# Optimization experiments

Hardware: AMD Instinct MI355X
Metric: run time of the kernel (lower is better)

The kernel has to match this reference:

```python
import jax, jax.numpy as jnp
import numpy as np

SIGMA = 1.0
TOP_K = 4

def setup_inputs() -> dict:
    key = jax.random.key(0)
    k1, k2, k3, k4 = jax.random.split(key, 4)
    B, N, IN_DIM, OUT_DIM, P = 2, 4096, 128, 128, 3
    x = jax.random.normal(k1, (B, N, IN_DIM), dtype=jnp.float32)
    pos = jax.random.normal(k2, (B, N, P), dtype=jnp.float32)
    # Linear(in_dim, out_dim): W [in_dim, out_dim], b [out_dim]
    lim = 1.0 / np.sqrt(IN_DIM)
    W = jax.random.uniform(k3, (IN_DIM, OUT_DIM), minval=-lim, maxval=lim, dtype=jnp.float32)
    b = jax.random.uniform(k4, (OUT_DIM,), minval=-lim, maxval=lim, dtype=jnp.float32)
    return {"x": x, "pos": pos, "W": W, "b": b}

def reference(x, pos, W, b):
    B, N, _ = x.shape
    # pairwise distances [B, N, N]
    pos_diff = pos[:, :, None, :] - pos[:, None, :, :]
    dist = jnp.sqrt(jnp.sum(pos_diff ** 2, axis=-1) + 1e-8)
    adj = jnp.exp(-dist ** 2 / (2.0 * SIGMA ** 2))
    # top-k mask along last dim
    _, indices = jax.lax.top_k(adj, TOP_K)  # [B, N, k]
    b_idx = jnp.arange(B)[:, None, None]
    n_idx = jnp.arange(N)[None, :, None]
    mask = jnp.zeros_like(adj).at[b_idx, n_idx, indices].set(1.0)
    adj = adj * mask
    adj = adj / (jnp.sum(adj, axis=-1, keepdims=True) + 1e-8)
    # weighted aggregation + linear
    out = jnp.einsum('bnm,bmd->bnd', adj, x)
    return out @ W + b
```

## Files before the change

kernel.cpp:

```cpp
#include <hip/hip_runtime.h>
#include <hip/hip_bf16.h>

#define NPTS 4096
#define NROWS 8192
#define DIM 128
#define GEMM_BLOCKS 1024
#define HCELL 0.25f
#define LOW (-4.0f)
#define CAP 16
#define NCELLS 32768
#define OVCAP 4096

typedef __attribute__((ext_vector_type(8))) short bf16x8;
typedef __attribute__((ext_vector_type(4))) float f32x4;

__device__ __forceinline__ int cellcoord(float v) {
    int c = (int)floorf((v - LOW) / HCELL);
    return c < 0 ? 0 : (c > 31 ? 31 : c);
}

__global__ __launch_bounds__(256) void k1_gemm_bin(const float* __restrict__ x,
        const float* __restrict__ pos, const float* __restrict__ W,
        __hip_bfloat16* __restrict__ xWb, unsigned* __restrict__ cellCnt,
        float4* __restrict__ cellPts, unsigned* __restrict__ ovfCnt,
        float4* __restrict__ ovfList) {
    int b = blockIdx.x;
    if (b >= GEMM_BLOCKS) {
        int t = (b - GEMM_BLOCKS) * 256 + threadIdx.x;
        int batch = t >> 12;
        const float* p = pos + (size_t)t * 3;
        float px = p[0], py = p[1], pz = p[2];
        int cx = cellcoord(px), cy = cellcoord(py), cz = cellcoord(pz);
        int cid = ((batch * 32 + cz) * 32 + cy) * 32 + cx;
        unsigned slot = atomicAdd(&cellCnt[cid], 1u);
        float4 rec = make_float4(px, py, pz, __uint_as_float((unsigned)(t & (NPTS - 1))));
        if (slot < CAP) cellPts[(size_t)cid * CAP + slot] = rec;
        else { unsigned o = atomicAdd(&ovfCnt[batch], 1u);
               if (o < OVCAP) ovfList[(size_t)batch * OVCAP + o] = rec; }
        return;
    }
    int wave = threadIdx.x >> 6, lane = threadIdx.x & 63;
    int tile = b * 4 + wave;
    int m0 = (tile >> 3) << 4, n0 = (tile & 7) << 4;
    int r = lane & 15, kg = lane >> 4;
    const float* xr = x + (size_t)(m0 + r) * DIM + kg * 8;
    const float* wc = W + (size_t)(kg * 8) * DIM + (n0 + r);
    f32x4 acc = {0.f, 0.f, 0.f, 0.f};
    union { __hip_bfloat16 h; short s; } u;
#pragma unroll
    for (int kb = 0; kb < 4; ++kb) {
        float4 a0 = *(const float4*)(xr + kb * 32);
        float4 a1 = *(const float4*)(xr + kb * 32 + 4);
        bf16x8 af, bf;
        u.h = __float2bfloat16(a0.x); af[0] = u.s;
        u.h = __float2bfloat16(a0.y); af[1] = u.s;
        u.h = __float2bfloat16(a0.z); af[2] = u.s;
        u.h = __float2bfloat16(a0.w); af[3] = u.s;
        u.h = __float2bfloat16(a1.x); af[4] = u.s;
        u.h = __float2bfloat16(a1.y); af[5] = u.s;
        u.h = __float2bfloat16(a1.z); af[6] = u.s;
        u.h = __float2bfloat16(a1.w); af[7] = u.s;
#pragma unroll
        for (int i = 0; i < 8; ++i) {
            u.h = __float2bfloat16(wc[(size_t)(kb * 32 + i) * DIM]);
            bf[i] = u.s;
        }
        acc = __builtin_amdgcn_mfma_f32_16x16x32_bf16(af, bf, acc, 0, 0, 0);
    }
    int col = n0 + r, rbase = m0 + (kg << 2);
#pragma unroll
    for (int reg = 0; reg < 4; ++reg)
        xWb[(size_t)(rbase + reg) * DIM + col] = __float2bfloat16(acc[reg]);
}

__device__ __forceinline__ double mkkey(float d2, int j) {
    return __longlong_as_double(__double_as_longlong((double)d2) |
                                (unsigned long long)(unsigned)j);
}
__device__ __forceinline__ void kins(double& k0, double& k1, double& k2,
                                     double& k3, double s) {
    double c = fmax(k0, s); k0 = fmin(k0, s);
    double t = fmax(k1, c); k1 = fmin(k1, c); c = t;
    t = fmax(k2, c);        k2 = fmin(k2, c); c = t;
    k3 = fmin(k3, c);
}
__device__ __forceinline__ void kmerge(double& a0, double& a1, double& a2,
                                       double& a3, double b0, double b1,
                                       double b2, double b3) {
    double m0 = fmin(a0, b3), m1 = fmin(a1, b2);
    double m2 = fmin(a2, b1), m3 = fmin(a3, b0);
    double t0 = fmin(m0, m2), t2 = fmax(m0, m2);
    double t1 = fmin(m1, m3), t3 = fmax(m1, m3);
    a0 = fmin(t0, t1); a1 = fmax(t0, t1);
    a2 = fmin(t2, t3); a3 = fmax(t2, t3);
}

__global__ __launch_bounds__(256) void knn_agg(const unsigned* __restrict__ cellCnt,
        const float4* __restrict__ cellPts, const unsigned* __restrict__ ovfCnt,
        const float4* __restrict__ ovfList, const float* __restrict__ pos,
        const __hip_bfloat16* __restrict__ xWb, const float* __restrict__ bias,
        float* __restrict__ out) {
    int lane = threadIdx.x & 63;
    int wave = threadIdx.x >> 6;
    int row = blockIdx.x * 4 + wave;
    int batch = row >> 12;
    int qi = row & (NPTS - 1);
    const float* pb = pos + (size_t)batch * NPTS * 3;
    float qx = pb[3 * qi], qy = pb[3 * qi + 1], qz = pb[3 * qi + 2];
    int cx = cellcoord(qx), cy = cellcoord(qy), cz = cellcoord(qz);
    const unsigned* cb = cellCnt + (size_t)batch * NCELLS;
    const float4* pb4 = cellPts + (size_t)batch * NCELLS * CAP;

    const double INF = __builtin_inf();
    double k0 = INF, k1 = INF, k2 = INF, k3 = INF;

#pragma unroll
    for (int mm = 0; mm < 2; ++mm) {
        int m = lane + mm * 64;
        if (m < 125) {
            int dz = m / 25 - 2, dy = (m / 5) % 5 - 2, dx = m % 5 - 2;
            int nx = cx + dx, ny = cy + dy, nz = cz + dz;
            if ((unsigned)nx < 32u && (unsigned)ny < 32u && (unsigned)nz < 32u) {
                int lid = (nz * 32 + ny) * 32 + nx;
                unsigned c = cb[lid]; c = c < CAP ? c : CAP;
                const float4* cp = pb4 + (size_t)lid * CAP;
                for (unsigned s = 0; s < c; ++s) {
                    float4 p = cp[s];
                    float ddx = qx - p.x, ddy = qy - p.y, ddz = qz - p.z;
                    float d2 = fmaf(ddx, ddx, fmaf(ddy, ddy, ddz * ddz));
                    kins(k0, k1, k2, k3, mkkey(d2, (int)__float_as_uint(p.w)));
                }
            }
        }
    }
#pragma unroll
    for (int off = 1; off < 64; off <<= 1) {
        double p0 = __shfl_xor(k0, off), p1 = __shfl_xor(k1, off);
        double p2 = __shfl_xor(k2, off), p3 = __shfl_xor(k3, off);
        kmerge(k0, k1, k2, k3, p0, p1, p2, p3);
    }

    float dbox = 1e30f;
    if (cx - 2 > 0)  dbox = fminf(dbox, qx - (LOW + (cx - 2) * HCELL));
    if (cx + 2 < 31) dbox = fminf(dbox, (LOW + (cx + 3) * HCELL) - qx);
    if (cy - 2 > 0)  dbox = fminf(dbox, qy - (LOW + (cy - 2) * HCELL));
    if (cy + 2 < 31) dbox = fminf(dbox, (LOW + (cy + 3) * HCELL) - qy);
    if (cz - 2 > 0)  dbox = fminf(dbox, qz - (LOW + (cz - 2) * HCELL));
    if (cz + 2 < 31) dbox = fminf(dbox, (LOW + (cz + 3) * HCELL) - qz);
    bool resolved = ((float)k3 < 0.999f * dbox * dbox) && ((float)k3 < 1e29f);

    if (!resolved) {
        k0 = INF; k1 = INF; k2 = INF; k3 = INF;
#pragma unroll 4
        for (int t = 0; t < NPTS / 64; ++t) {
            int j = t * 64 + lane;
            float px = pb[3 * j], py = pb[3 * j + 1], pz = pb[3 * j + 2];
            float ddx = qx - px, ddy = qy - py, ddz = qz - pz;
            float d2 = fmaf(ddx, ddx, fmaf(ddy, ddy, ddz * ddz));
            kins(k0, k1, k2, k3, mkkey(d2, j));
        }
#pragma unroll
        for (int off = 1; off < 64; off <<= 1) {
            double p0 = __shfl_xor(k0, off), p1 = __shfl_xor(k1, off);
            double p2 = __shfl_xor(k2, off), p3 = __shfl_xor(k3, off);
            kmerge(k0, k1, k2, k3, p0, p1, p2, p3);
        }
    } else {
        unsigned oc = ovfCnt[batch]; oc = oc < OVCAP ? oc : OVCAP;
        const float4* ol = ovfList + (size_t)batch * OVCAP;
        for (unsigned o = 0; o < oc; ++o) {
            float4 p = ol[o];
            float ddx = qx - p.x, ddy = qy - p.y, ddz = qz - p.z;
            float d2 = fmaf(ddx, ddx, fmaf(ddy, ddy, ddz * ddz));
            kins(k0, k1, k2, k3, mkkey(d2, (int)__float_as_uint(p.w)));
        }
    }

    unsigned i0 = (unsigned)__double_as_longlong(k0) & 0xFFFu;
    unsigned i1 = (unsigned)__double_as_longlong(k1) & 0xFFFu;
    unsigned i2 = (unsigned)__double_as_longlong(k2) & 0xFFFu;
    unsigned i3 = (unsigned)__double_as_longlong(k3) & 0xFFFu;
    float d0 = (float)k0, d1 = (float)k1, d2 = (float)k2, d3 = (float)k3;
    float w0 = __expf(-(d0 + 1e-8f) * 0.5f);
    float w1 = __expf(-(d1 + 1e-8f) * 0.5f);
    float w2 = __expf(-(d2 + 1e-8f) * 0.5f);
    float w3 = __expf(-(d3 + 1e-8f) * 0.5f);
    float inv = 1.0f / (w0 + w1 + w2 + w3 + 1e-8f);
    w0 *= inv; w1 *= inv; w2 *= inv; w3 *= inv;
    int c = lane << 1;
    float2 bb = *(const float2*)(bias + c);
    const unsigned short* xu = (const unsigned short*)xWb;
    size_t bbase = ((size_t)batch * NPTS) << 7;
    ushort2 g0 = *(const ushort2*)(xu + bbase + ((size_t)i0 << 7) + c);
    ushort2 g1 = *(const ushort2*)(xu + bbase + ((size_t)i1 << 7) + c);
    ushort2 g2 = *(const ushort2*)(xu + bbase + ((size_t)i2 << 7) + c);
    ushort2 g3 = *(const ushort2*)(xu + bbase + ((size_t)i3 << 7) + c);
    float ox = bb.x + w0 * __uint_as_float((unsigned)g0.x << 16)
                    + w1 * __uint_as_float((unsigned)g1.x << 16)
                    + w2 * __uint_as_float((unsigned)g2.x << 16)
                    + w3 * __uint_as_float((unsigned)g3.x << 16);
    float oy = bb.y + w0 * __uint_as_float((unsigned)g0.y << 16)
                    + w1 * __uint_as_float((unsigned)g1.y << 16)
                    + w2 * __uint_as_float((unsigned)g2.y << 16)
                    + w3 * __uint_as_float((unsigned)g3.y << 16);
    *(float2*)(out + ((size_t)row << 7) + c) = make_float2(ox, oy);
}

extern "C" void kernel_launch(void* const* d_in, const int* in_sizes, int n_in,
                              void* d_out, int out_size, void* d_ws, size_t ws_size,
                              hipStream_t stream) {
    const float* x    = (const float*)d_in[0];
    const float* pos  = (const float*)d_in[1];
    const float* W    = (const float*)d_in[2];
    const float* bias = (const float*)d_in[3];
    float* out = (float*)d_out;

    char* ws = (char*)d_ws;
    __hip_bfloat16* xWb = (__hip_bfloat16*)ws;
    unsigned* cellCnt  = (unsigned*)(ws + 2097152);
    unsigned* ovfCnt   = (unsigned*)(ws + 2359296);
    float4* cellPts    = (float4*)(ws + 2359312);
    float4* ovfList    = (float4*)(ws + 2359312 + 16777216);

    hipMemsetAsync(ws + 2097152, 0, 262160, stream);
    k1_gemm_bin<<<GEMM_BLOCKS + NROWS / 256, 256, 0, stream>>>(
        x, pos, W, xWb, cellCnt, cellPts, ovfCnt, ovfList);
    knn_agg<<<NROWS / 4, 256, 0, stream>>>(
        cellCnt, cellPts, ovfCnt, ovfList, pos, xWb, bias, out);
}
```

Before: 84.27 us.

## Assign one block per query row and split cell scans across threads

The kNN kernel now processes one query row per 256-thread block instead of one per wave. Each of the 125 neighbour cells is split across two threads (half a cell each), with an inner loop unrolled by four, and per-wave top-4 results are merged through shared memory. This is meant to shorten the serial per-lane cell scan and expose more parallelism, at the cost of four times more blocks, two __syncthreads per merge, and half the threads idle in the output gather. The brute-force fallback is spread over 256 threads.

```diff
diff --git a/kernel.cpp b/kernel.cpp
--- a/kernel.cpp
+++ b/kernel.cpp
@@ -95,14 +95,37 @@
     a2 = fmin(t2, t3); a3 = fmax(t2, t3);
 }
 
+__device__ __forceinline__ void wave_bfly(double& k0, double& k1,
+                                          double& k2, double& k3) {
+#pragma unroll
+    for (int off = 1; off < 64; off <<= 1) {
+        double p0 = __shfl_xor(k0, off), p1 = __shfl_xor(k1, off);
+        double p2 = __shfl_xor(k2, off), p3 = __shfl_xor(k3, off);
+        kmerge(k0, k1, k2, k3, p0, p1, p2, p3);
+    }
+}
+
+__device__ __forceinline__ void block_merge(double (*sk)[4], int wave, int lane,
+                                            double& k0, double& k1,
+                                            double& k2, double& k3) {
+    __syncthreads();
+    if (lane == 0) { sk[wave][0] = k0; sk[wave][1] = k1;
+                     sk[wave][2] = k2; sk[wave][3] = k3; }
+    __syncthreads();
+    k0 = sk[0][0]; k1 = sk[0][1]; k2 = sk[0][2]; k3 = sk[0][3];
+    kmerge(k0, k1, k2, k3, sk[1][0], sk[1][1], sk[1][2], sk[1][3]);
+    kmerge(k0, k1, k2, k3, sk[2][0], sk[2][1], sk[2][2], sk[2][3]);
+    kmerge(k0, k1, k2, k3, sk[3][0], sk[3][1], sk[3][2], sk[3][3]);
+}
+
 __global__ __launch_bounds__(256) void knn_agg(const unsigned* __restrict__ cellCnt,
         const float4* __restrict__ cellPts, const unsigned* __restrict__ ovfCnt,
         const float4* __restrict__ ovfList, const float* __restrict__ pos,
         const __hip_bfloat16* __restrict__ xWb, const float* __restrict__ bias,
         float* __restrict__ out) {
-    int lane = threadIdx.x & 63;
-    int wave = threadIdx.x >> 6;
-    int row = blockIdx.x * 4 + wave;
+    int t = threadIdx.x;
+    int lane = t & 63, wave = t >> 6;
+    int row = blockIdx.x;
     int batch = row >> 12;
     int qi = row & (NPTS - 1);
     const float* pb = pos + (size_t)batch * NPTS * 3;
@@ -111,34 +134,47 @@
     const unsigned* cb = cellCnt + (size_t)batch * NCELLS;
     const float4* pb4 = cellPts + (size_t)batch * NCELLS * CAP;
 
+    __shared__ double sk[4][4];
+
     const double INF = __builtin_inf();
     double k0 = INF, k1 = INF, k2 = INF, k3 = INF;
 
-#pragma unroll
-    for (int mm = 0; mm < 2; ++mm) {
-        int m = lane + mm * 64;
-        if (m < 125) {
-            int dz = m / 25 - 2, dy = (m / 5) % 5 - 2, dx = m % 5 - 2;
-            int nx = cx + dx, ny = cy + dy, nz = cz + dz;
-            if ((unsigned)nx < 32u && (unsigned)ny < 32u && (unsigned)nz < 32u) {
-                int lid = (nz * 32 + ny) * 32 + nx;
-                unsigned c = cb[lid]; c = c < CAP ? c : CAP;
-                const float4* cp = pb4 + (size_t)lid * CAP;
-                for (unsigned s = 0; s < c; ++s) {
-                    float4 p = cp[s];
-                    float ddx = qx - p.x, ddy = qy - p.y, ddz = qz - p.z;
-                    float d2 = fmaf(ddx, ddx, fmaf(ddy, ddy, ddz * ddz));
-                    kins(k0, k1, k2, k3, mkkey(d2, (int)__float_as_uint(p.w)));
-                }
+    int m = t >> 1, h = t & 1;
+    if (m < 125) {
+        int dz = m / 25 - 2, dy = (m / 5) % 5 - 2, dx = m % 5 - 2;
+        int nx = cx + dx, ny = cy + dy, nz = cz + dz;
+        if ((unsigned)nx < 32u && (unsigned)ny < 32u && (unsigned)nz < 32u) {
+            int lid = (nz * 32 + ny) * 32 + nx;
+            unsigned c = cb[lid]; c = c < CAP ? c : CAP;
+            int lo = h << 3;
+            int hi = (int)c < lo + 8 ? (int)c : lo + 8;
+            const float4* cp = pb4 + (size_t)lid * CAP;
+            int s = lo;
+            for (; s + 3 < hi; s += 4) {
+                float4 p0 = cp[s], p1 = cp[s + 1], p2 = cp[s + 2], p3 = cp[s + 3];
+                float dx0 = qx - p0.x, dy0 = qy - p0.y, dz0 = qz - p0.z;
+                float dx1 = qx - p1.x, dy1 = qy - p1.y, dz1 = qz - p1.z;
+                float dx2 = qx - p2.x, dy2 = qy - p2.y, dz2 = qz - p2.z;
+                float dx3 = qx - p3.x, dy3 = qy - p3.y, dz3 = qz - p3.z;
+                float e0 = fmaf(dx0, dx0, fmaf(dy0, dy0, dz0 * dz0));
+                float e1 = fmaf(dx1, dx1, fmaf(dy1, dy1, dz1 * dz1));
+                float e2 = fmaf(dx2, dx2, fmaf(dy2, dy2, dz2 * dz2));
+                float e3 = fmaf(dx3, dx3, fmaf(dy3, dy3, dz3 * dz3));
+                kins(k0, k1, k2, k3, mkkey(e0, (int)__float_as_uint(p0.w)));
+                kins(k0, k1, k2, k3, mkkey(e1, (int)__float_as_uint(p1.w)));
+                kins(k0, k1, k2, k3, mkkey(e2, (int)__float_as_uint(p2.w)));
+                kins(k0, k1, k2, k3, mkkey(e3, (int)__float_as_uint(p3.w)));
             }
-        }
-    }
-#pragma unroll
-    for (int off = 1; off < 64; off <<= 1) {
-        double p0 = __shfl_xor(k0, off), p1 = __shfl_xor(k1, off);
-        double p2 = __shfl_xor(k2, off), p3 = __shfl_xor(k3, off);
-        kmerge(k0, k1, k2, k3, p0, p1, p2, p3);
-    }
+            for (; s < hi; ++s) {
+                float4 p = cp[s];
+                float ddx = qx - p.x, ddy = qy - p.y, ddz = qz - p.z;
+                float d2 = fmaf(ddx, ddx, fmaf(ddy, ddy, ddz * ddz));
+                kins(k0, k1, k2, k3, mkkey(d2, (int)__float_as_uint(p.w)));
+            }
+        }
+    }
+    wave_bfly(k0, k1, k2, k3);
+    block_merge(sk, wave, lane, k0, k1, k2, k3);
 
     float dbox = 1e30f;
     if (cx - 2 > 0)  dbox = fminf(dbox, qx - (LOW + (cx - 2) * HCELL));
@@ -152,19 +188,15 @@
     if (!resolved) {
         k0 = INF; k1 = INF; k2 = INF; k3 = INF;
 #pragma unroll 4
-        for (int t = 0; t < NPTS / 64; ++t) {
-            int j = t * 64 + lane;
+        for (int it = 0; it < NPTS / 256; ++it) {
+            int j = (it << 8) + t;
             float px = pb[3 * j], py = pb[3 * j + 1], pz = pb[3 * j + 2];
             float ddx = qx - px, ddy = qy - py, ddz = qz - pz;
             float d2 = fmaf(ddx, ddx, fmaf(ddy, ddy, ddz * ddz));
             kins(k0, k1, k2, k3, mkkey(d2, j));
         }
-#pragma unroll
-        for (int off = 1; off < 64; off <<= 1) {
-            double p0 = __shfl_xor(k0, off), p1 = __shfl_xor(k1, off);
-            double p2 = __shfl_xor(k2, off), p3 = __shfl_xor(k3, off);
-            kmerge(k0, k1, k2, k3, p0, p1, p2, p3);
-        }
+        wave_bfly(k0, k1, k2, k3);
+        block_merge(sk, wave, lane, k0, k1, k2, k3);
     } else {
         unsigned oc = ovfCnt[batch]; oc = oc < OVCAP ? oc : OVCAP;
         const float4* ol = ovfList + (size_t)batch * OVCAP;
@@ -187,23 +219,16 @@
     float w3 = __expf(-(d3 + 1e-8f) * 0.5f);
     float inv = 1.0f / (w0 + w1 + w2 + w3 + 1e-8f);
     w0 *= inv; w1 *= inv; w2 *= inv; w3 *= inv;
-    int c = lane << 1;
-    float2 bb = *(const float2*)(bias + c);
-    const unsigned short* xu = (const unsigned short*)xWb;
-    size_t bbase = ((size_t)batch * NPTS) << 7;
-    ushort2 g0 = *(const ushort2*)(xu + bbase + ((size_t)i0 << 7) + c);
-    ushort2 g1 = *(const ushort2*)(xu + bbase + ((size_t)i1 << 7) + c);
-    ushort2 g2 = *(const ushort2*)(xu + bbase + ((size_t)i2 << 7) + c);
-    ushort2 g3 = *(const ushort2*)(xu + bbase + ((size_t)i3 << 7) + c);
-    float ox = bb.x + w0 * __uint_as_float((unsigned)g0.x << 16)
-                    + w1 * __uint_as_float((unsigned)g1.x << 16)
-                    + w2 * __uint_as_float((unsigned)g2.x << 16)
-                    + w3 * __uint_as_float((unsigned)g3.x << 16);
-    float oy = bb.y + w0 * __uint_as_float((unsigned)g0.y << 16)
-                    + w1 * __uint_as_float((unsigned)g1.y << 16)
-                    + w2 * __uint_as_float((unsigned)g2.y << 16)
-                    + w3 * __uint_as_float((unsigned)g3.y << 16);
-    *(float2*)(out + ((size_t)row << 7) + c) = make_float2(ox, oy);
+    if (t < DIM) {
+        const unsigned short* xu = (const unsigned short*)xWb;
+        size_t bbase = ((size_t)batch * NPTS) << 7;
+        float g0 = __uint_as_float((unsigned)xu[bbase + ((size_t)i0 << 7) + t] << 16);
+        float g1 = __uint_as_float((unsigned)xu[bbase + ((size_t)i1 << 7) + t] << 16);
+        float g2 = __uint_as_float((unsigned)xu[bbase + ((size_t)i2 << 7) + t] << 16);
+        float g3 = __uint_as_float((unsigned)xu[bbase + ((size_t)i3 << 7) + t] << 16);
+        out[((size_t)row << 7) + t] =
+            bias[t] + w0 * g0 + w1 * g1 + w2 * g2 + w3 * g3;
+    }
 }
 
 extern "C" void kernel_launch(void* const* d_in, const int* in_sizes, int n_in,
@@ -225,6 +250,6 @@
     hipMemsetAsync(ws + 2097152, 0, 262160, stream);
     k1_gemm_bin<<<GEMM_BLOCKS + NROWS / 256, 256, 0, stream>>>(
         x, pos, W, xWb, cellCnt, cellPts, ovfCnt, ovfList);
-    knn_agg<<<NROWS / 4, 256, 0, stream>>>(
+    knn_agg<<<NROWS, 256, 0, stream>>>(
         cellCnt, cellPts, ovfCnt, ovfList, pos, xWb, bias, out);
 }
```

Result: slower. 96.79 us (+14.8%).

## Search 3x3x3 cell neighborhood first, fall back to 5x5x5 then brute force

Applied to the files above, without the earlier changes.

The kNN search now scans the 27 surrounding cells first, with two lanes per cell each handling half of the cell's slots and a 4-way unrolled inner loop. It then checks whether the 4th-nearest distance is inside the 3x3x3 box bound. Only unresolved queries fall back to the previous 5x5x5 scan and then to the brute-force pass. This avoids scanning 125 cells with uneven per-lane loops for most queries, at the cost of an extra wave reduction and duplicated work for queries that need the fallback.

```diff
diff --git a/kernel.cpp b/kernel.cpp
--- a/kernel.cpp
+++ b/kernel.cpp
@@ -94,6 +94,15 @@
     a0 = fmin(t0, t1); a1 = fmax(t0, t1);
     a2 = fmin(t2, t3); a3 = fmax(t2, t3);
 }
+__device__ __forceinline__ void wave_bfly(double& k0, double& k1,
+                                          double& k2, double& k3) {
+#pragma unroll
+    for (int off = 1; off < 64; off <<= 1) {
+        double p0 = __shfl_xor(k0, off), p1 = __shfl_xor(k1, off);
+        double p2 = __shfl_xor(k2, off), p3 = __shfl_xor(k3, off);
+        kmerge(k0, k1, k2, k3, p0, p1, p2, p3);
+    }
+}
 
 __global__ __launch_bounds__(256) void knn_agg(const unsigned* __restrict__ cellCnt,
         const float4* __restrict__ cellPts, const unsigned* __restrict__ ovfCnt,
@@ -114,58 +123,99 @@
     const double INF = __builtin_inf();
     double k0 = INF, k1 = INF, k2 = INF, k3 = INF;
 
-#pragma unroll
-    for (int mm = 0; mm < 2; ++mm) {
-        int m = lane + mm * 64;
-        if (m < 125) {
-            int dz = m / 25 - 2, dy = (m / 5) % 5 - 2, dx = m % 5 - 2;
-            int nx = cx + dx, ny = cy + dy, nz = cz + dz;
-            if ((unsigned)nx < 32u && (unsigned)ny < 32u && (unsigned)nz < 32u) {
-                int lid = (nz * 32 + ny) * 32 + nx;
-                unsigned c = cb[lid]; c = c < CAP ? c : CAP;
-                const float4* cp = pb4 + (size_t)lid * CAP;
-                for (unsigned s = 0; s < c; ++s) {
-                    float4 p = cp[s];
-                    float ddx = qx - p.x, ddy = qy - p.y, ddz = qz - p.z;
-                    float d2 = fmaf(ddx, ddx, fmaf(ddy, ddy, ddz * ddz));
-                    kins(k0, k1, k2, k3, mkkey(d2, (int)__float_as_uint(p.w)));
+    int m = lane >> 1, h = lane & 1;
+    if (m < 27) {
+        int dz = m / 9 - 1, dy = (m / 3) % 3 - 1, dx = m % 3 - 1;
+        int nx = cx + dx, ny = cy + dy, nz = cz + dz;
+        if ((unsigned)nx < 32u && (unsigned)ny < 32u && (unsigned)nz < 32u) {
+            int lid = (nz * 32 + ny) * 32 + nx;
+            unsigned c = cb[lid]; c = c < CAP ? c : CAP;
+            int lo = h << 3;
+            int hi = (int)c < lo + 8 ? (int)c : lo + 8;
+            const float4* cp = pb4 + (size_t)lid * CAP;
+            int s = lo;
+            for (; s + 3 < hi; s += 4) {
+                float4 p0 = cp[s], p1 = cp[s + 1], p2 = cp[s + 2], p3 = cp[s + 3];
+                float dx0 = qx - p0.x, dy0 = qy - p0.y, dz0 = qz - p0.z;
+                float dx1 = qx - p1.x, dy1 = qy - p1.y, dz1 = qz - p1.z;
+                float dx2 = qx - p2.x, dy2 = qy - p2.y, dz2 = qz - p2.z;
+                float dx3 = qx - p3.x, dy3 = qy - p3.y, dz3 = qz - p3.z;
+                float e0 = fmaf(dx0, dx0, fmaf(dy0, dy0, dz0 * dz0));
+                float e1 = fmaf(dx1, dx1, fmaf(dy1, dy1, dz1 * dz1));
+                float e2 = fmaf(dx2, dx2, fmaf(dy2, dy2, dz2 * dz2));
+                float e3 = fmaf(dx3, dx3, fmaf(dy3, dy3, dz3 * dz3));
+                kins(k0, k1, k2, k3, mkkey(e0, (int)__float_as_uint(p0.w)));
+                kins(k0, k1, k2, k3, mkkey(e1, (int)__float_as_uint(p1.w)));
+                kins(k0, k1, k2, k3, mkkey(e2, (int)__float_as_uint(p2.w)));
+                kins(k0, k1, k2, k3, mkkey(e3, (int)__float_as_uint(p3.w)));
+            }
+            for (; s < hi; ++s) {
+                float4 p = cp[s];
+                float ddx = qx - p.x, ddy = qy - p.y, ddz = qz - p.z;
+                float d2 = fmaf(ddx, ddx, fmaf(ddy, ddy, ddz * ddz));
+                kins(k0, k1, k2, k3, mkkey(d2, (int)__float_as_uint(p.w)));
+            }
+        }
+    }
+    wave_bfly(k0, k1, k2, k3);
+
+    float db1 = 1e30f;
+    if (cx - 1 > 0)  db1 = fminf(db1, qx - (LOW + (cx - 1) * HCELL));
+    if (cx + 1 < 31) db1 = fminf(db1, (LOW + (cx + 2) * HCELL) - qx);
+    if (cy - 1 > 0)  db1 = fminf(db1, qy - (LOW + (cy - 1) * HCELL));
+    if (cy + 1 < 31) db1 = fminf(db1, (LOW + (cy + 2) * HCELL) - qy);
+    if (cz - 1 > 0)  db1 = fminf(db1, qz - (LOW + (cz - 1) * HCELL));
+    if (cz + 1 < 31) db1 = fminf(db1, (LOW + (cz + 2) * HCELL) - qz);
+    bool res1 = ((float)k3 < 0.999f * db1 * db1) && ((float)k3 < 1e29f);
+    bool res2 = false;
+
+    if (!res1) {
+        k0 = INF; k1 = INF; k2 = INF; k3 = INF;
+#pragma unroll
+        for (int mm = 0; mm < 2; ++mm) {
+            int m2 = lane + mm * 64;
+            if (m2 < 125) {
+                int dz = m2 / 25 - 2, dy = (m2 / 5) % 5 - 2, dx = m2 % 5 - 2;
+                int nx = cx + dx, ny = cy + dy, nz = cz + dz;
+                if ((unsigned)nx < 32u && (unsigned)ny < 32u && (unsigned)nz < 32u) {
+                    int lid = (nz * 32 + ny) * 32 + nx;
+                    unsigned c = cb[lid]; c = c < CAP ? c : CAP;
+                    const float4* cp = pb4 + (size_t)lid * CAP;
+                    for (unsigned s = 0; s < c; ++s) {
+                        float4 p = cp[s];
+                        float ddx = qx - p.x, ddy = qy - p.y, ddz = qz - p.z;
+                        float d2 = fmaf(ddx, ddx, fmaf(ddy, ddy, ddz * ddz));
+                        kins(k0, k1, k2, k3, mkkey(d2, (int)__float_as_uint(p.w)));
+                    }
                 }
             }
         }
-    }
-#pragma unroll
-    for (int off = 1; off < 64; off <<= 1) {
-        double p0 = __shfl_xor(k0, off), p1 = __shfl_xor(k1, off);
-        double p2 = __shfl_xor(k2, off), p3 = __shfl_xor(k3, off);
-        kmerge(k0, k1, k2, k3, p0, p1, p2, p3);
-    }
-
-    float dbox = 1e30f;
-    if (cx - 2 > 0)  dbox = fminf(dbox, qx - (LOW + (cx - 2) * HCELL));
-    if (cx + 2 < 31) dbox = fminf(dbox, (LOW + (cx + 3) * HCELL) - qx);
-    if (cy - 2 > 0)  dbox = fminf(dbox, qy - (LOW + (cy - 2) * HCELL));
-    if (cy + 2 < 31) dbox = fminf(dbox, (LOW + (cy + 3) * HCELL) - qy);
-    if (cz - 2 > 0)  dbox = fminf(dbox, qz - (LOW + (cz - 2) * HCELL));
-    if (cz + 2 < 31) dbox = fminf(dbox, (LOW + (cz + 3) * HCELL) - qz);
-    bool resolved = ((float)k3 < 0.999f * dbox * dbox) && ((float)k3 < 1e29f);
-
-    if (!resolved) {
-        k0 = INF; k1 = INF; k2 = INF; k3 = INF;
+        wave_bfly(k0, k1, k2, k3);
+
+        float dbox = 1e30f;
+        if (cx - 2 > 0)  dbox = fminf(dbox, qx - (LOW + (cx - 2) * HCELL));
+        if (cx + 2 < 31) dbox = fminf(dbox, (LOW + (cx + 3) * HCELL) - qx);
+        if (cy - 2 > 0)  dbox = fminf(dbox, qy - (LOW + (cy - 2) * HCELL));
+        if (cy + 2 < 31) dbox = fminf(dbox, (LOW + (cy + 3) * HCELL) - qy);
+        if (cz - 2 > 0)  dbox = fminf(dbox, qz - (LOW + (cz - 2) * HCELL));
+        if (cz + 2 < 31) dbox = fminf(dbox, (LOW + (cz + 3) * HCELL) - qz);
+        res2 = ((float)k3 < 0.999f * dbox * dbox) && ((float)k3 < 1e29f);
+
+        if (!res2) {
+            k0 = INF; k1 = INF; k2 = INF; k3 = INF;
 #pragma unroll 4
-        for (int t = 0; t < NPTS / 64; ++t) {
-            int j = t * 64 + lane;
-            float px = pb[3 * j], py = pb[3 * j + 1], pz = pb[3 * j + 2];
-            float ddx = qx - px, ddy = qy - py, ddz = qz - pz;
-            float d2 = fmaf(ddx, ddx, fmaf(ddy, ddy, ddz * ddz));
-            kins(k0, k1, k2, k3, mkkey(d2, j));
-        }
-#pragma unroll
-        for (int off = 1; off < 64; off <<= 1) {
-            double p0 = __shfl_xor(k0, off), p1 = __shfl_xor(k1, off);
-            double p2 = __shfl_xor(k2, off), p3 = __shfl_xor(k3, off);
-            kmerge(k0, k1, k2, k3, p0, p1, p2, p3);
-        }
-    } else {
+            for (int t = 0; t < NPTS / 64; ++t) {
+                int j = t * 64 + lane;
+                float px = pb[3 * j], py = pb[3 * j + 1], pz = pb[3 * j + 2];
+                float ddx = qx - px, ddy = qy - py, ddz = qz - pz;
+                float d2 = fmaf(ddx, ddx, fmaf(ddy, ddy, ddz * ddz));
+                kins(k0, k1, k2, k3, mkkey(d2, j));
+            }
+            wave_bfly(k0, k1, k2, k3);
+        }
+    }
+
+    if (res1 || res2) {
         unsigned oc = ovfCnt[batch]; oc = oc < OVCAP ? oc : OVCAP;
         const float4* ol = ovfList + (size_t)batch * OVCAP;
         for (unsigned o = 0; o < oc; ++o) {
```

New measurement: 86.01 us. 2.1% more time.

## Split cell scans across half-slots with dual top-4 accumulators

Applied to the files above, without the earlier changes.

Each of the 125 neighbor cells is now scanned by two lanes, each handling half of the 16 slots, which spreads the per-cell work over 250 lane tasks. Slot loads are unrolled by four. Two independent top-4 lists are kept to shorten the dependency chain of the insertion network, and they are merged before the wave butterfly. The brute-force fallback also uses two accumulators. This adds more loads of cell counts and extra registers, which may lower occupancy.

```diff
diff --git a/kernel.cpp b/kernel.cpp
--- a/kernel.cpp
+++ b/kernel.cpp
@@ -94,6 +94,15 @@
     a0 = fmin(t0, t1); a1 = fmax(t0, t1);
     a2 = fmin(t2, t3); a3 = fmax(t2, t3);
 }
+__device__ __forceinline__ void wave_bfly(double& k0, double& k1,
+                                          double& k2, double& k3) {
+#pragma unroll
+    for (int off = 1; off < 64; off <<= 1) {
+        double p0 = __shfl_xor(k0, off), p1 = __shfl_xor(k1, off);
+        double p2 = __shfl_xor(k2, off), p3 = __shfl_xor(k3, off);
+        kmerge(k0, k1, k2, k3, p0, p1, p2, p3);
+    }
+}
 
 __global__ __launch_bounds__(256) void knn_agg(const unsigned* __restrict__ cellCnt,
         const float4* __restrict__ cellPts, const unsigned* __restrict__ ovfCnt,
@@ -113,32 +122,58 @@
 
     const double INF = __builtin_inf();
     double k0 = INF, k1 = INF, k2 = INF, k3 = INF;
-
-#pragma unroll
-    for (int mm = 0; mm < 2; ++mm) {
-        int m = lane + mm * 64;
-        if (m < 125) {
-            int dz = m / 25 - 2, dy = (m / 5) % 5 - 2, dx = m % 5 - 2;
-            int nx = cx + dx, ny = cy + dy, nz = cz + dz;
-            if ((unsigned)nx < 32u && (unsigned)ny < 32u && (unsigned)nz < 32u) {
-                int lid = (nz * 32 + ny) * 32 + nx;
-                unsigned c = cb[lid]; c = c < CAP ? c : CAP;
-                const float4* cp = pb4 + (size_t)lid * CAP;
-                for (unsigned s = 0; s < c; ++s) {
-                    float4 p = cp[s];
-                    float ddx = qx - p.x, ddy = qy - p.y, ddz = qz - p.z;
-                    float d2 = fmaf(ddx, ddx, fmaf(ddy, ddy, ddz * ddz));
-                    kins(k0, k1, k2, k3, mkkey(d2, (int)__float_as_uint(p.w)));
-                }
-            }
-        }
-    }
-#pragma unroll
-    for (int off = 1; off < 64; off <<= 1) {
-        double p0 = __shfl_xor(k0, off), p1 = __shfl_xor(k1, off);
-        double p2 = __shfl_xor(k2, off), p3 = __shfl_xor(k3, off);
-        kmerge(k0, k1, k2, k3, p0, p1, p2, p3);
-    }
+    double l0 = INF, l1 = INF, l2 = INF, l3 = INF;
+
+    int lids[4], cnts[4];
+#pragma unroll
+    for (int uu = 0; uu < 4; ++uu) {
+        int u = lane + (uu << 6);
+        int cell = u < 125 ? u : u - 125;
+        int dzz = cell / 25 - 2, dyy = (cell / 5) % 5 - 2, dxx = cell % 5 - 2;
+        int nx = cx + dxx, ny = cy + dyy, nz = cz + dzz;
+        bool ok = (u < 250) && ((unsigned)nx < 32u) &&
+                  ((unsigned)ny < 32u) && ((unsigned)nz < 32u);
+        int lid = ok ? ((nz * 32 + ny) * 32 + nx) : 0;
+        lids[uu] = lid;
+        cnts[uu] = ok ? (int)cb[lid] : 0;
+    }
+
+    auto scan_half = [&](int uu, double& s0, double& s1, double& s2, double& s3) {
+        int u = lane + (uu << 6);
+        int h = u < 125 ? 0 : 1;
+        int c = cnts[uu]; c = c < CAP ? c : CAP;
+        int lo = h << 3;
+        int hi = c < lo + 8 ? c : lo + 8;
+        const float4* cp = pb4 + (size_t)lids[uu] * CAP;
+        int sl = lo;
+        for (; sl + 3 < hi; sl += 4) {
+            float4 p0 = cp[sl], p1 = cp[sl + 1], p2 = cp[sl + 2], p3 = cp[sl + 3];
+            float dx0 = qx - p0.x, dy0 = qy - p0.y, dz0 = qz - p0.z;
+            float dx1 = qx - p1.x, dy1 = qy - p1.y, dz1 = qz - p1.z;
+            float dx2 = qx - p2.x, dy2 = qy - p2.y, dz2 = qz - p2.z;
+            float dx3 = qx - p3.x, dy3 = qy - p3.y, dz3 = qz - p3.z;
+            float e0 = fmaf(dx0, dx0, fmaf(dy0, dy0, dz0 * dz0));
+            float e1 = fmaf(dx1, dx1, fmaf(dy1, dy1, dz1 * dz1));
+            float e2 = fmaf(dx2, dx2, fmaf(dy2, dy2, dz2 * dz2));
+            float e3 = fmaf(dx3, dx3, fmaf(dy3, dy3, dz3 * dz3));
+            kins(s0, s1, s2, s3, mkkey(e0, (int)__float_as_uint(p0.w)));
+            kins(s0, s1, s2, s3, mkkey(e1, (int)__float_as_uint(p1.w)));
+            kins(s0, s1, s2, s3, mkkey(e2, (int)__float_as_uint(p2.w)));
+            kins(s0, s1, s2, s3, mkkey(e3, (int)__float_as_uint(p3.w)));
+        }
+        for (; sl < hi; ++sl) {
+            float4 p = cp[sl];
+            float ddx = qx - p.x, ddy = qy - p.y, ddz = qz - p.z;
+            float d2 = fmaf(ddx, ddx, fmaf(ddy, ddy, ddz * ddz));
+            kins(s0, s1, s2, s3, mkkey(d2, (int)__float_as_uint(p.w)));
+        }
+    };
+    scan_half(0, k0, k1, k2, k3);
+    scan_half(1, l0, l1, l2, l3);
+    scan_half(2, k0, k1, k2, k3);
+    scan_half(3, l0, l1, l2, l3);
+    kmerge(k0, k1, k2, k3, l0, l1, l2, l3);
+    wave_bfly(k0, k1, k2, k3);
 
     float dbox = 1e30f;
     if (cx - 2 > 0)  dbox = fminf(dbox, qx - (LOW + (cx - 2) * HCELL));
@@ -151,20 +186,22 @@
 
     if (!resolved) {
         k0 = INF; k1 = INF; k2 = INF; k3 = INF;
+        l0 = INF; l1 = INF; l2 = INF; l3 = INF;
 #pragma unroll 4
-        for (int t = 0; t < NPTS / 64; ++t) {
-            int j = t * 64 + lane;
-            float px = pb[3 * j], py = pb[3 * j + 1], pz = pb[3 * j + 2];
-            float ddx = qx - px, ddy = qy - py, ddz = qz - pz;
-            float d2 = fmaf(ddx, ddx, fmaf(ddy, ddy, ddz * ddz));
-            kins(k0, k1, k2, k3, mkkey(d2, j));
-        }
-#pragma unroll
-        for (int off = 1; off < 64; off <<= 1) {
-            double p0 = __shfl_xor(k0, off), p1 = __shfl_xor(k1, off);
-            double p2 = __shfl_xor(k2, off), p3 = __shfl_xor(k3, off);
-            kmerge(k0, k1, k2, k3, p0, p1, p2, p3);
-        }
+        for (int tt = 0; tt < 32; ++tt) {
+            int j0 = (tt << 7) + lane;
+            int j1 = j0 + 64;
+            float px0 = pb[3 * j0], py0 = pb[3 * j0 + 1], pz0 = pb[3 * j0 + 2];
+            float px1 = pb[3 * j1], py1 = pb[3 * j1 + 1], pz1 = pb[3 * j1 + 2];
+            float dx0 = qx - px0, dy0 = qy - py0, dz0 = qz - pz0;
+            float dx1 = qx - px1, dy1 = qy - py1, dz1 = qz - pz1;
+            float d20 = fmaf(dx0, dx0, fmaf(dy0, dy0, dz0 * dz0));
+            float d21 = fmaf(dx1, dx1, fmaf(dy1, dy1, dz1 * dz1));
+            kins(k0, k1, k2, k3, mkkey(d20, j0));
+            kins(l0, l1, l2, l3, mkkey(d21, j1));
+        }
+        kmerge(k0, k1, k2, k3, l0, l1, l2, l3);
+        wave_bfly(k0, k1, k2, k3);
     } else {
         unsigned oc = ovfCnt[batch]; oc = oc < OVCAP ? oc : OVCAP;
         const float4* ol = ovfList + (size_t)batch * OVCAP;
```

After: 86.59 us. 1.03x slower.
